# Kernel tuning notes

Measured on AMD Instinct MI355X. Metric: run time of the kernel, lower is better.

The kernel has to match this reference:

```python
import jax, jax.numpy as jnp
import numpy as np

N_NODES = 200000
N_EDGES = 3200000
F_IN, HID, N_CLS = 128, 35, 10


def setup_inputs() -> dict:
    key = jax.random.key(0)
    k = jax.random.split(key, 5)
    x = jax.random.normal(k[0], (N_NODES, F_IN), dtype=jnp.float32)
    edge_index = jax.random.randint(k[1], (2, N_EDGES), 0, N_NODES, dtype=jnp.int64)
    W1 = jax.random.normal(k[2], (F_IN, HID), dtype=jnp.float32) / np.sqrt(F_IN)
    b1 = jnp.zeros((HID,), dtype=jnp.float32)
    W2 = jax.random.normal(k[3], (HID, N_CLS), dtype=jnp.float32) / np.sqrt(HID)
    b2 = jnp.zeros((N_CLS,), dtype=jnp.float32)
    return {"x": x, "edge_index": edge_index, "W1": W1, "b1": b1, "W2": W2, "b2": b2}


def _gcn_conv(x, W, b, row, col, norm, n_nodes):
    # GCNConv: linear transform, then normalized neighbor aggregation (scatter-add)
    h = x @ W                               # [N, d_out]
    msg = h[row] * norm[:, None]            # gather along edges, [E+N, d_out]
    agg = jax.ops.segment_sum(msg, col, num_segments=n_nodes)
    return agg + b


def reference(x, edge_index, W1, b1, W2, b2):
    n = x.shape[0]
    loop = jnp.arange(n, dtype=edge_index.dtype)
    row = jnp.concatenate([edge_index[0], loop])  # sources (+ self loops)
    col = jnp.concatenate([edge_index[1], loop])  # targets (+ self loops)
    deg = jax.ops.segment_sum(jnp.ones_like(col, dtype=x.dtype), col, num_segments=n)
    dinv = jnp.where(deg > 0, deg ** -0.5, 0.0)
    norm = dinv[row] * dinv[col]                  # D^{-1/2} A D^{-1/2} edge weights

    h = _gcn_conv(x, W1, b1, row, col, norm, n)
    h = jax.nn.relu(h)
    # F.dropout with training=self.training: identity at inference
    out = _gcn_conv(h, W2, b2, row, col, norm, n)
    return jax.nn.log_softmax(out, axis=1)
```

## Files before the change

kernel.cpp:

```cpp
#include <hip/hip_runtime.h>

#define NN    200000
#define F_IN  128
#define HID   35
#define NCLS  10
#define LD1   36
#define LD2   12
#define NPB   256
#define NB    782
#define CAP   5120
#define EPT   32

static __device__ inline unsigned short f2bf(float f) {
    unsigned u = __float_as_uint(f);
    u = (u + 0x7FFFu + ((u >> 16) & 1u)) >> 16;
    return (unsigned short)u;
}
static __device__ inline unsigned pk2(float a, float b) {
    return (unsigned)f2bf(a) | ((unsigned)f2bf(b) << 16);
}
static __device__ inline float bf2f(unsigned short h) {
    return __uint_as_float((unsigned)h << 16);
}


__global__ void k_initcur(int* __restrict__ gcur) {
    int t = threadIdx.x;
    if (t < NB) gcur[t] = t * CAP;
}

__global__ __launch_bounds__(256)
void k_bucket(const int* __restrict__ row, const int* __restrict__ col, int E,
              int* __restrict__ gcur, unsigned* __restrict__ bkt) {
    __shared__ int hist[NB];
    __shared__ int basev[NB];
    int t = threadIdx.x;
    long e0 = (long)blockIdx.x * (256 * EPT);
    for (int i = t; i < NB; i += 256) hist[i] = 0;
    __syncthreads();
    int cols[EPT];
#pragma unroll
    for (int i = 0; i < EPT; ++i) {
        long e = e0 + (long)i * 256 + t;
        if (e < E) {
            int c = col[e];
            cols[i] = c;
            atomicAdd(&hist[c >> 8], 1);
        } else cols[i] = -1;
    }
    __syncthreads();
    for (int i = t; i < NB; i += 256) {
        int h = hist[i];
        basev[i] = (h > 0) ? atomicAdd(&gcur[i], h) : 0;
        hist[i] = 0;
    }
    __syncthreads();
#pragma unroll
    for (int i = 0; i < EPT; ++i) {
        int c = cols[i];
        if (c >= 0) {
            long e = e0 + (long)i * 256 + t;
            int r = row[e];
            int b = c >> 8;
            int pos = basev[b] + atomicAdd(&hist[b], 1);
            if (pos < NB * CAP) bkt[pos] = (unsigned)r | ((unsigned)(c & 255) << 18);
        }
    }
}

__global__ __launch_bounds__(256)
void k_sort(unsigned* __restrict__ bkt, const int* __restrict__ gcur,
            int* __restrict__ obeg, int* __restrict__ oend,
            float* __restrict__ dinv, int n) {
    __shared__ unsigned est[CAP];
    __shared__ int hist[NPB];
    __shared__ int cur[NPB];
    __shared__ int sc[NPB];
    int b = blockIdx.x, t = threadIdx.x;
    int ec = gcur[b] - b * CAP;
    if (ec > CAP) ec = CAP;
    unsigned* ep = bkt + (size_t)b * CAP;
    hist[t] = 0;
    __syncthreads();
    for (int e = t; e < ec; e += 256) {
        unsigned p = ep[e];
        est[e] = p;
        atomicAdd(&hist[p >> 18], 1);
    }
    __syncthreads();
    sc[t] = hist[t];
    __syncthreads();
    for (int d = 1; d < NPB; d <<= 1) {
        int add = (t >= d) ? sc[t - d] : 0;
        __syncthreads();
        sc[t] += add;
        __syncthreads();
    }
    int excl = sc[t] - hist[t];
    cur[t] = excl;
    int i = b * NPB + t;
    if (i < n) {
        obeg[i] = b * CAP + excl;
        oend[i] = b * CAP + excl + hist[t];
        dinv[i] = rsqrtf((float)(hist[t] + 1));
    }
    __syncthreads();
    for (int e = t; e < ec; e += 256) {
        unsigned p = est[e];
        int lc = p >> 18;
        int pos = atomicAdd(&cur[lc], 1);
        ep[pos] = p & 0x3FFFF;
    }
}


__global__ void k_gemm1(const float* __restrict__ x, const float* __restrict__ W1,
                        const float* __restrict__ dinv, unsigned short* __restrict__ hs1b,
                        int n) {
    int i = blockIdx.x * blockDim.x + threadIdx.x;
    if (i >= n) return;
    float acc[HID];
#pragma unroll
    for (int j = 0; j < HID; ++j) acc[j] = 0.f;
    const float4* xr = (const float4*)(x + (size_t)i * F_IN);
    for (int k4 = 0; k4 < F_IN / 4; ++k4) {
        float4 xv = xr[k4];
        const float* w = W1 + (size_t)(k4 * 4) * HID;
#pragma unroll
        for (int j = 0; j < HID; ++j)
            acc[j] += xv.x * w[j] + xv.y * w[HID + j] + xv.z * w[2 * HID + j] + xv.w * w[3 * HID + j];
    }
    float d = dinv[i];
    unsigned* o32 = (unsigned*)(hs1b + (size_t)i * LD1);
#pragma unroll
    for (int j = 0; j < 17; ++j) o32[j] = pk2(acc[2 * j] * d, acc[2 * j + 1] * d);
    o32[17] = pk2(acc[34] * d, 0.f);
}

__global__ void k_agg1(const int* __restrict__ obeg, const int* __restrict__ oend,
                       const unsigned* __restrict__ srow,
                       const unsigned short* __restrict__ hs1b,
                       float* __restrict__ acc1, int n) {
    int wid = (blockIdx.x * blockDim.x + threadIdx.x) >> 6;
    int lane = threadIdx.x & 63;
    if (wid >= n) return;
    int beg = obeg[wid], end = oend[wid];
    bool act = lane < LD1;
    float acc = 0.f;
    if (act) acc = bf2f(hs1b[(size_t)wid * LD1 + lane]);
    int j = beg;
    for (; j + 3 < end; j += 4) {
        int r0 = srow[j], r1 = srow[j + 1], r2 = srow[j + 2], r3 = srow[j + 3];
        float a0 = 0.f, a1 = 0.f, a2 = 0.f, a3 = 0.f;
        if (act) {
            a0 = bf2f(hs1b[(size_t)r0 * LD1 + lane]);
            a1 = bf2f(hs1b[(size_t)r1 * LD1 + lane]);
            a2 = bf2f(hs1b[(size_t)r2 * LD1 + lane]);
            a3 = bf2f(hs1b[(size_t)r3 * LD1 + lane]);
        }
        acc += (a0 + a1) + (a2 + a3);
    }
    for (; j < end; ++j) {
        int r = srow[j];
        if (act) acc += bf2f(hs1b[(size_t)r * LD1 + lane]);
    }
    if (act) acc1[(size_t)wid * LD1 + lane] = acc;
}


__global__ void k_layer2(const float* __restrict__ acc1, const float* __restrict__ dinv,
                         const float* __restrict__ b1, const float* __restrict__ W2,
                         unsigned short* __restrict__ hs2b, int n) {
    int i = blockIdx.x * blockDim.x + threadIdx.x;
    if (i >= n) return;
    float d = dinv[i];
    const float4* a = (const float4*)(acc1 + (size_t)i * LD1);
    float4 tq[9];
#pragma unroll
    for (int q = 0; q < 9; ++q) tq[q] = a[q];
    const float* tf = (const float*)tq;
    float h[HID];
#pragma unroll
    for (int k = 0; k < HID; ++k) {
        float v = tf[k] * d + b1[k];
        h[k] = v > 0.f ? v : 0.f;
    }
    float o[NCLS];
#pragma unroll
    for (int j = 0; j < NCLS; ++j) o[j] = 0.f;
#pragma unroll
    for (int k = 0; k < HID; ++k) {
#pragma unroll
        for (int j = 0; j < NCLS; ++j) o[j] += h[k] * W2[k * NCLS + j];
    }
    unsigned* dst = (unsigned*)(hs2b + (size_t)i * LD2);
#pragma unroll
    for (int j = 0; j < 5; ++j) dst[j] = pk2(o[2 * j] * d, o[2 * j + 1] * d);
    dst[5] = 0u;
}

__global__ void k_agg2(const int* __restrict__ obeg, const int* __restrict__ oend,
                       const unsigned* __restrict__ srow,
                       const unsigned short* __restrict__ hs2b,
                       float* __restrict__ acc2, int n) {
    int wid = (blockIdx.x * blockDim.x + threadIdx.x) >> 6;
    int lane = threadIdx.x & 63;
    if (wid >= n) return;
    int sub = lane >> 4;
    int f = lane & 15;
    bool act = f < LD2;
    int beg = obeg[wid], end = oend[wid];
    float acc = 0.f;
    if (lane < LD2) acc = bf2f(hs2b[(size_t)wid * LD2 + lane]);
    for (int j = beg + sub; j < end; j += 4) {
        int r = srow[j];
        if (act) acc += bf2f(hs2b[(size_t)r * LD2 + f]);
    }
    acc += __shfl_down(acc, 32);
    acc += __shfl_down(acc, 16);
    if (lane < LD2) acc2[(size_t)wid * LD2 + lane] = acc;
}

__global__ void k_out(const float* __restrict__ acc2, const float* __restrict__ dinv,
                      const float* __restrict__ b2, float* __restrict__ out, int n) {
    int i = blockIdx.x * blockDim.x + threadIdx.x;
    if (i >= n) return;
    float d = dinv[i];
    const float4* a = (const float4*)(acc2 + (size_t)i * LD2);
    float4 t0 = a[0], t1 = a[1], t2 = a[2];
    float v[NCLS] = {t0.x, t0.y, t0.z, t0.w, t1.x, t1.y, t1.z, t1.w, t2.x, t2.y};
    float m = -1e30f;
#pragma unroll
    for (int j = 0; j < NCLS; ++j) {
        v[j] = v[j] * d + b2[j];
        m = fmaxf(m, v[j]);
    }
    float s = 0.f;
#pragma unroll
    for (int j = 0; j < NCLS; ++j) s += expf(v[j] - m);
    float l = logf(s);
    float* o = out + (size_t)i * NCLS;
#pragma unroll
    for (int j = 0; j < NCLS; ++j) o[j] = v[j] - m - l;
}

extern "C" void kernel_launch(void* const* d_in, const int* in_sizes, int n_in,
                              void* d_out, int out_size, void* d_ws, size_t ws_size,
                              hipStream_t stream) {
    const float* x  = (const float*)d_in[0];
    const int*   ei = (const int*)d_in[1];
    const float* W1 = (const float*)d_in[2];
    const float* b1 = (const float*)d_in[3];
    const float* W2 = (const float*)d_in[4];
    const float* b2 = (const float*)d_in[5];
    float* out = (float*)d_out;

    const int n = in_sizes[0] / F_IN;
    const int E = in_sizes[1] / 2;
    const int* row = ei;
    const int* col = ei + E;

    unsigned*       bkt  = (unsigned*)d_ws;
    int*            gcur = (int*)d_ws + 4003840;
    int*            obeg = (int*)d_ws + 4004864;
    int*            oend = (int*)d_ws + 4204864;
    float*          dinv = (float*)d_ws + 4404864;
    unsigned short* hs1b = (unsigned short*)((unsigned*)d_ws + 4604864);
    float*          acc1 = (float*)d_ws + 8204864;
    unsigned short* hs2b = hs1b;
    float*          acc2 = (float*)d_ws + 5804864;

    const int B = 256;
    const int nbk = (E + B * EPT - 1) / (B * EPT);

    k_initcur<<<1, 1024, 0, stream>>>(gcur);
    k_bucket<<<nbk, B, 0, stream>>>(row, col, E, gcur, bkt);
    k_sort<<<NB, B, 0, stream>>>(bkt, gcur, obeg, oend, dinv, n);

    k_gemm1<<<(n + B - 1) / B, B, 0, stream>>>(x, W1, dinv, hs1b, n);
    k_agg1<<<(n * 64 + B - 1) / B, B, 0, stream>>>(obeg, oend, bkt, hs1b, acc1, n);
    k_layer2<<<(n + B - 1) / B, B, 0, stream>>>(acc1, dinv, b1, W2, hs2b, n);
    k_agg2<<<(n * 64 + B - 1) / B, B, 0, stream>>>(obeg, oend, bkt, hs2b, acc2, n);
    k_out<<<(n + B - 1) / B, B, 0, stream>>>(acc2, dinv, b2, out, n);
}
```

Before: 365.5 us.

## Split layer-1 features into 32+4 arrays, half-wave edges, fuse agg2 with softmax

Layer-1 features are now stored in two bf16 arrays: a 64-byte block holding features 0-31 and an 8-byte block holding 32-35. This lets each half-wavefront gather a whole 64-byte row for alternate edges, instead of a 72-byte row in which 28 lanes sit idle, and the two halves are combined with a shuffle. The second aggregation kernel now applies log-softmax with 16-lane shuffles and writes the output directly, which removes the acc2 round trip and one launch. The cost is an extra scattered small load per edge for the 4-feature tail array.

```diff
diff --git a/kernel.cpp b/kernel.cpp
--- a/kernel.cpp
+++ b/kernel.cpp
@@ -3,9 +3,9 @@
 #define NN    200000
 #define F_IN  128
 #define HID   35
-#define NCLS  10
 #define LD1   36
 #define LD2   12
+#define NCLS  10
 #define NPB   256
 #define NB    782
 #define CAP   5120
@@ -115,8 +115,9 @@
 
 
 __global__ void k_gemm1(const float* __restrict__ x, const float* __restrict__ W1,
-                        const float* __restrict__ dinv, unsigned short* __restrict__ hs1b,
-                        int n) {
+                        const float* __restrict__ dinv,
+                        unsigned short* __restrict__ hs1A,
+                        unsigned short* __restrict__ hs1B, int n) {
     int i = blockIdx.x * blockDim.x + threadIdx.x;
     if (i >= n) return;
     float acc[HID];
@@ -131,40 +132,53 @@
             acc[j] += xv.x * w[j] + xv.y * w[HID + j] + xv.z * w[2 * HID + j] + xv.w * w[3 * HID + j];
     }
     float d = dinv[i];
-    unsigned* o32 = (unsigned*)(hs1b + (size_t)i * LD1);
-#pragma unroll
-    for (int j = 0; j < 17; ++j) o32[j] = pk2(acc[2 * j] * d, acc[2 * j + 1] * d);
-    o32[17] = pk2(acc[34] * d, 0.f);
+    unsigned* oa = (unsigned*)(hs1A + (size_t)i * 32);
+#pragma unroll
+    for (int j = 0; j < 16; ++j) oa[j] = pk2(acc[2 * j] * d, acc[2 * j + 1] * d);
+    unsigned* ob = (unsigned*)(hs1B + (size_t)i * 4);
+    ob[0] = pk2(acc[32] * d, acc[33] * d);
+    ob[1] = pk2(acc[34] * d, 0.f);
 }
 
 __global__ void k_agg1(const int* __restrict__ obeg, const int* __restrict__ oend,
                        const unsigned* __restrict__ srow,
-                       const unsigned short* __restrict__ hs1b,
+                       const unsigned short* __restrict__ A,
+                       const unsigned short* __restrict__ Bf,
                        float* __restrict__ acc1, int n) {
     int wid = (blockIdx.x * blockDim.x + threadIdx.x) >> 6;
     int lane = threadIdx.x & 63;
     if (wid >= n) return;
+    int half = lane >> 5;
+    int fl = lane & 31;
+    bool bact = fl < 4;
     int beg = obeg[wid], end = oend[wid];
-    bool act = lane < LD1;
-    float acc = 0.f;
-    if (act) acc = bf2f(hs1b[(size_t)wid * LD1 + lane]);
-    int j = beg;
-    for (; j + 3 < end; j += 4) {
-        int r0 = srow[j], r1 = srow[j + 1], r2 = srow[j + 2], r3 = srow[j + 3];
-        float a0 = 0.f, a1 = 0.f, a2 = 0.f, a3 = 0.f;
-        if (act) {
-            a0 = bf2f(hs1b[(size_t)r0 * LD1 + lane]);
-            a1 = bf2f(hs1b[(size_t)r1 * LD1 + lane]);
-            a2 = bf2f(hs1b[(size_t)r2 * LD1 + lane]);
-            a3 = bf2f(hs1b[(size_t)r3 * LD1 + lane]);
+    float acc  = (half == 0) ? bf2f(A[(size_t)wid * 32 + fl]) : 0.f;
+    float accb = (half == 0 && bact) ? bf2f(Bf[(size_t)wid * 4 + fl]) : 0.f;
+    int j = beg + half;
+    for (; j + 6 < end; j += 8) {
+        int r0 = srow[j], r1 = srow[j + 2], r2 = srow[j + 4], r3 = srow[j + 6];
+        float a0 = bf2f(A[(size_t)r0 * 32 + fl]);
+        float a1 = bf2f(A[(size_t)r1 * 32 + fl]);
+        float a2 = bf2f(A[(size_t)r2 * 32 + fl]);
+        float a3 = bf2f(A[(size_t)r3 * 32 + fl]);
+        acc += (a0 + a1) + (a2 + a3);
+        if (bact) {
+            float b0 = bf2f(Bf[(size_t)r0 * 4 + fl]);
+            float b1 = bf2f(Bf[(size_t)r1 * 4 + fl]);
+            float b2v = bf2f(Bf[(size_t)r2 * 4 + fl]);
+            float b3 = bf2f(Bf[(size_t)r3 * 4 + fl]);
+            accb += (b0 + b1) + (b2v + b3);
         }
-        acc += (a0 + a1) + (a2 + a3);
-    }
-    for (; j < end; ++j) {
+    }
+    for (; j < end; j += 2) {
         int r = srow[j];
-        if (act) acc += bf2f(hs1b[(size_t)r * LD1 + lane]);
-    }
-    if (act) acc1[(size_t)wid * LD1 + lane] = acc;
+        acc += bf2f(A[(size_t)r * 32 + fl]);
+        if (bact) accb += bf2f(Bf[(size_t)r * 4 + fl]);
+    }
+    acc  += __shfl_xor(acc, 32);
+    accb += __shfl_xor(accb, 32);
+    if (lane < 32) acc1[(size_t)wid * LD1 + lane] = acc;
+    if (lane < 4)  acc1[(size_t)wid * LD1 + 32 + lane] = accb;
 }
 
 
@@ -199,10 +213,11 @@
     dst[5] = 0u;
 }
 
-__global__ void k_agg2(const int* __restrict__ obeg, const int* __restrict__ oend,
-                       const unsigned* __restrict__ srow,
-                       const unsigned short* __restrict__ hs2b,
-                       float* __restrict__ acc2, int n) {
+__global__ void k_agg2o(const int* __restrict__ obeg, const int* __restrict__ oend,
+                        const unsigned* __restrict__ srow,
+                        const unsigned short* __restrict__ hs2b,
+                        const float* __restrict__ dinv, const float* __restrict__ b2,
+                        float* __restrict__ out, int n) {
     int wid = (blockIdx.x * blockDim.x + threadIdx.x) >> 6;
     int lane = threadIdx.x & 63;
     if (wid >= n) return;
@@ -210,38 +225,27 @@
     int f = lane & 15;
     bool act = f < LD2;
     int beg = obeg[wid], end = oend[wid];
-    float acc = 0.f;
-    if (lane < LD2) acc = bf2f(hs2b[(size_t)wid * LD2 + lane]);
+    float acc = (lane < LD2) ? bf2f(hs2b[(size_t)wid * LD2 + lane]) : 0.f;
     for (int j = beg + sub; j < end; j += 4) {
         int r = srow[j];
         if (act) acc += bf2f(hs2b[(size_t)r * LD2 + f]);
     }
     acc += __shfl_down(acc, 32);
     acc += __shfl_down(acc, 16);
-    if (lane < LD2) acc2[(size_t)wid * LD2 + lane] = acc;
-}
-
-__global__ void k_out(const float* __restrict__ acc2, const float* __restrict__ dinv,
-                      const float* __restrict__ b2, float* __restrict__ out, int n) {
-    int i = blockIdx.x * blockDim.x + threadIdx.x;
-    if (i >= n) return;
-    float d = dinv[i];
-    const float4* a = (const float4*)(acc2 + (size_t)i * LD2);
-    float4 t0 = a[0], t1 = a[1], t2 = a[2];
-    float v[NCLS] = {t0.x, t0.y, t0.z, t0.w, t1.x, t1.y, t1.z, t1.w, t2.x, t2.y};
-    float m = -1e30f;
-#pragma unroll
-    for (int j = 0; j < NCLS; ++j) {
-        v[j] = v[j] * d + b2[j];
-        m = fmaxf(m, v[j]);
-    }
-    float s = 0.f;
-#pragma unroll
-    for (int j = 0; j < NCLS; ++j) s += expf(v[j] - m);
-    float l = logf(s);
-    float* o = out + (size_t)i * NCLS;
-#pragma unroll
-    for (int j = 0; j < NCLS; ++j) o[j] = v[j] - m - l;
+    float d = dinv[wid];
+    float v = (lane < NCLS) ? acc * d + b2[lane] : -1e30f;
+    float m = v;
+    m = fmaxf(m, __shfl_xor(m, 1, 16));
+    m = fmaxf(m, __shfl_xor(m, 2, 16));
+    m = fmaxf(m, __shfl_xor(m, 4, 16));
+    m = fmaxf(m, __shfl_xor(m, 8, 16));
+    float e = (lane < NCLS) ? expf(v - m) : 0.f;
+    float s = e;
+    s += __shfl_xor(s, 1, 16);
+    s += __shfl_xor(s, 2, 16);
+    s += __shfl_xor(s, 4, 16);
+    s += __shfl_xor(s, 8, 16);
+    if (lane < NCLS) out[(size_t)wid * NCLS + lane] = v - m - logf(s);
 }
 
 extern "C" void kernel_launch(void* const* d_in, const int* in_sizes, int n_in,
@@ -265,10 +269,10 @@
     int*            obeg = (int*)d_ws + 4004864;
     int*            oend = (int*)d_ws + 4204864;
     float*          dinv = (float*)d_ws + 4404864;
-    unsigned short* hs1b = (unsigned short*)((unsigned*)d_ws + 4604864);
+    unsigned short* hs1A = (unsigned short*)((unsigned*)d_ws + 4604864);
+    unsigned short* hs1B = (unsigned short*)((unsigned*)d_ws + 7804864);
     float*          acc1 = (float*)d_ws + 8204864;
-    unsigned short* hs2b = hs1b;
-    float*          acc2 = (float*)d_ws + 5804864;
+    unsigned short* hs2b = hs1A;
 
     const int B = 256;
     const int nbk = (E + B * EPT - 1) / (B * EPT);
@@ -277,9 +281,8 @@
     k_bucket<<<nbk, B, 0, stream>>>(row, col, E, gcur, bkt);
     k_sort<<<NB, B, 0, stream>>>(bkt, gcur, obeg, oend, dinv, n);
 
-    k_gemm1<<<(n + B - 1) / B, B, 0, stream>>>(x, W1, dinv, hs1b, n);
-    k_agg1<<<(n * 64 + B - 1) / B, B, 0, stream>>>(obeg, oend, bkt, hs1b, acc1, n);
+    k_gemm1<<<(n + B - 1) / B, B, 0, stream>>>(x, W1, dinv, hs1A, hs1B, n);
+    k_agg1<<<(n * 64 + B - 1) / B, B, 0, stream>>>(obeg, oend, bkt, hs1A, hs1B, acc1, n);
     k_layer2<<<(n + B - 1) / B, B, 0, stream>>>(acc1, dinv, b1, W2, hs2b, n);
-    k_agg2<<<(n * 64 + B - 1) / B, B, 0, stream>>>(obeg, oend, bkt, hs2b, acc2, n);
-    k_out<<<(n + B - 1) / B, B, 0, stream>>>(acc2, dinv, b2, out, n);
-}
+    k_agg2o<<<(n * 64 + B - 1) / B, B, 0, stream>>>(obeg, oend, bkt, hs2b, dinv, b2, out, n);
+}
```

Measured after the change: 372.2 us. Within noise of the previous version (+1.8%).
